# Optimization experiments

Measured on AMD Instinct MI355X. Metric: run time of the kernel, lower is better.

## Reference

```python
import jax, jax.numpy as jnp
import numpy as np

B, S, E = 4, 2048, 1024
H, Dh = 16, 64


def setup_inputs() -> dict:
    key = jax.random.key(0)
    ks = jax.random.split(key, 9)
    scale_in = 1.0 / np.sqrt(E)
    scale_out = 1.0 / np.sqrt(H * Dh)
    x = jax.random.normal(ks[0], (B, S, E), dtype=jnp.float32)
    # Per-head projection weights stacked over heads: [H, E, Dh]
    Wq = jax.random.uniform(ks[1], (H, E, Dh), jnp.float32, -scale_in, scale_in)
    bq = jax.random.uniform(ks[2], (H, Dh), jnp.float32, -scale_in, scale_in)
    Wk = jax.random.uniform(ks[3], (H, E, Dh), jnp.float32, -scale_in, scale_in)
    bk = jax.random.uniform(ks[4], (H, Dh), jnp.float32, -scale_in, scale_in)
    Wv = jax.random.uniform(ks[5], (H, E, Dh), jnp.float32, -scale_in, scale_in)
    bv = jax.random.uniform(ks[6], (H, Dh), jnp.float32, -scale_in, scale_in)
    # Output projection: [H*Dh, E]
    Wo = jax.random.uniform(ks[7], (H * Dh, E), jnp.float32, -scale_out, scale_out)
    bo = jax.random.uniform(ks[8], (E,), jnp.float32, -scale_out, scale_out)
    return {"x": x, "Wq": Wq, "bq": bq, "Wk": Wk, "bk": bk,
            "Wv": Wv, "bv": bv, "Wo": Wo, "bo": bo}


def reference(x, Wq, bq, Wk, bk, Wv, bv, Wo, bo):
    # Per-head linear projections, batched over heads: [B, H, S, Dh]
    q = jnp.einsum('bse,hed->bhsd', x, Wq) + bq[None, :, None, :]
    k = jnp.einsum('bse,hed->bhsd', x, Wk) + bk[None, :, None, :]
    v = jnp.einsum('bse,hed->bhsd', x, Wv) + bv[None, :, None, :]
    scale = 1.0 / jnp.sqrt(jnp.asarray(Dh, dtype=x.dtype))
    scores = jnp.einsum('bhsd,bhtd->bhst', q, k) * scale  # [B, H, S, S]
    weights = jax.nn.softmax(scores, axis=-1)
    z = jnp.einsum('bhst,bhtd->bhsd', weights, v)  # [B, H, S, Dh]
    # Concat heads in module order: [B, S, H*Dh]
    z = jnp.transpose(z, (0, 2, 1, 3)).reshape(B, S, H * Dh)
    return z @ Wo + bo
```

## Files before the change

kernel.cpp:

```cpp
#include <hip/hip_runtime.h>
#include <hip/hip_bf16.h>

#define B_  4
#define S_  2048
#define E_  1024
#define H_  16
#define DH_ 64
#define M_  (B_*S_)
#define HD_ (H_*DH_)

typedef unsigned short u16;
typedef __attribute__((ext_vector_type(8))) __bf16 bf16x8;
typedef __attribute__((ext_vector_type(4))) __bf16 bf16x4;
typedef __attribute__((ext_vector_type(4))) float  f32x4;

#if __has_builtin(__builtin_amdgcn_exp2f)
#define EXP2F __builtin_amdgcn_exp2f
#else
#define EXP2F __builtin_exp2f
#endif

#define QSCALE 0.18033688011112042f

__device__ __forceinline__ void g2l16(const void* g, void* l) {
  __builtin_amdgcn_global_load_lds(
      (const __attribute__((address_space(1))) void*)g,
      (__attribute__((address_space(3))) void*)l, 16, 0, 0);
}

__device__ __forceinline__ u16 f2bf(float f) {
  union { float f; unsigned u; } v; v.f = f;
  unsigned r = v.u + 0x7FFFu + ((v.u >> 16) & 1u);
  return (u16)(r >> 16);
}

__global__ __launch_bounds__(256) void prep_kernel(
    const float* __restrict__ x, const float* __restrict__ Wq,
    const float* __restrict__ Wk, const float* __restrict__ Wv,
    const float* __restrict__ Wo,
    u16* __restrict__ xb, u16* __restrict__ wqkvT, u16* __restrict__ woT) {
  __shared__ u16 tile[64][66];
  const int blk = blockIdx.x, tid = threadIdx.x;
  if (blk < 8192) {
    int i = blk * 256 + tid;
    float4 v = ((const float4*)x)[i];
    ushort4 o;
    o.x = f2bf(v.x); o.y = f2bf(v.y); o.z = f2bf(v.z); o.w = f2bf(v.w);
    ((ushort4*)xb)[i] = o;
  } else if (blk < 8960) {
    int b2 = blk - 8192;
    int p = b2 >> 8, h = (b2 >> 4) & 15, e0 = (b2 & 15) * 64;
    const float* src = (p == 0 ? Wq : (p == 1 ? Wk : Wv)) + h * (E_ * DH_);
#pragma unroll
    for (int r = 0; r < 16; ++r) {
      int idx = r * 256 + tid;
      int el = idx >> 6, d = idx & 63;
      tile[el][d] = f2bf(src[(e0 + el) * DH_ + d]);
    }
    __syncthreads();
    u16* dst = wqkvT + (p * HD_ + h * DH_) * E_;
#pragma unroll
    for (int r = 0; r < 16; ++r) {
      int idx = r * 256 + tid;
      int d = idx >> 6, el = idx & 63;
      dst[d * E_ + e0 + el] = tile[el][d];
    }
  } else {
    int b3 = blk - 8960;
    int c0 = (b3 >> 4) * 64, e0 = (b3 & 15) * 64;
#pragma unroll
    for (int r = 0; r < 16; ++r) {
      int idx = r * 256 + tid;
      int cl = idx >> 6, el = idx & 63;
      tile[cl][el] = f2bf(Wo[(c0 + cl) * E_ + e0 + el]);
    }
    __syncthreads();
#pragma unroll
    for (int r = 0; r < 16; ++r) {
      int idx = r * 256 + tid;
      int er = idx >> 6, cl = idx & 63;
      woT[(e0 + er) * HD_ + c0 + cl] = tile[cl][er];
    }
  }
}

__global__ __launch_bounds__(256) void gemm_qkv_kernel(
    const u16* __restrict__ A, const u16* __restrict__ Bt,
    const float* __restrict__ b0, const float* __restrict__ b1,
    const float* __restrict__ b2,
    u16* __restrict__ oQ, u16* __restrict__ oK, u16* __restrict__ oV) {
  constexpr int K = 1024;
  __shared__ __align__(16) u16 smem[2 * 128 * 64];
  u16* As = smem;
  u16* Bs = smem + 128 * 64;
  const int tid = threadIdx.x;
  const int lane = tid & 63, wv = tid >> 6;
  const int wm = (wv >> 1) * 64, wn = (wv & 1) * 64;
  const int q4 = lane >> 4, lm = lane & 15;
  const int tileM = blockIdx.y * 128, tileN = blockIdx.x * 128;

  const u16* gA[4]; const u16* gB[4]; u16* lA[4]; u16* lB[4];
#pragma unroll
  for (int rr = 0; rr < 4; ++rr) {
    int c = rr * 256 + tid;
    int r = c >> 3, sw = ((c & 7) ^ (r & 7)) * 8;
    gA[rr] = A + (size_t)(tileM + r) * K + sw;
    gB[rr] = Bt + (size_t)(tileN + r) * K + sw;
    lA[rr] = As + c * 8;
    lB[rr] = Bs + c * 8;
  }

  f32x4 acc[4][4] = {};

  int aoff[2][4], boff[2][4];
#pragma unroll
  for (int ks = 0; ks < 2; ++ks) {
#pragma unroll
    for (int i = 0; i < 4; ++i) {
      int ra = wm + i * 16 + lm;
      aoff[ks][i] = ra * 64 + (((ks * 4 + q4) ^ (ra & 7)) * 8);
      int rb = wn + i * 16 + lm;
      boff[ks][i] = rb * 64 + (((ks * 4 + q4) ^ (rb & 7)) * 8);
    }
  }

  for (int k0 = 0; k0 < K; k0 += 64) {
#pragma unroll
    for (int rr = 0; rr < 4; ++rr) {
      g2l16(gA[rr] + k0, lA[rr]);
      g2l16(gB[rr] + k0, lB[rr]);
    }
    __syncthreads();
#pragma unroll
    for (int ks = 0; ks < 2; ++ks) {
      bf16x8 af[4], bf[4];
#pragma unroll
      for (int i = 0; i < 4; ++i) af[i] = *(const bf16x8*)(As + aoff[ks][i]);
#pragma unroll
      for (int j = 0; j < 4; ++j) bf[j] = *(const bf16x8*)(Bs + boff[ks][j]);
#pragma unroll
      for (int i = 0; i < 4; ++i)
#pragma unroll
        for (int j = 0; j < 4; ++j)
          acc[i][j] = __builtin_amdgcn_mfma_f32_16x16x32_bf16(af[i], bf[j], acc[i][j], 0, 0, 0);
    }
    __syncthreads();
  }

  u16* TT = smem;
  const int ccb = tileN & 1023;
  const int proj = tileN >> 10;
  const float scl = (proj == 0 ? QSCALE : 1.0f);
  const float* bp = (proj == 0 ? b0 : (proj == 1 ? b1 : b2));
#pragma unroll
  for (int j = 0; j < 4; ++j) {
    int ncl = wn + j * 16 + lm;
    float bs = bp[ccb + ncl];
#pragma unroll
    for (int i = 0; i < 4; ++i) {
      int m0 = wm + i * 16 + q4 * 4;
      f32x4 vv;
#pragma unroll
      for (int r = 0; r < 4; ++r) vv[r] = (acc[i][j][r] + bs) * scl;
      bf16x4 ov = __builtin_convertvector(vv, bf16x4);
      if (proj < 2) {
        ushort4 us = *(ushort4*)&ov;
        TT[(m0 + 0) * 128 + (ncl ^ (8 * ((m0 + 0) & 15)))] = us.x;
        TT[(m0 + 1) * 128 + (ncl ^ (8 * ((m0 + 1) & 15)))] = us.y;
        TT[(m0 + 2) * 128 + (ncl ^ (8 * ((m0 + 2) & 15)))] = us.z;
        TT[(m0 + 3) * 128 + (ncl ^ (8 * ((m0 + 3) & 15)))] = us.w;
      } else {
        *(bf16x4*)(TT + ncl * 128 + (m0 ^ (8 * (ncl & 15)))) = ov;
      }
    }
  }
  __syncthreads();
  if (proj < 2) {
    u16* optr = (proj == 0 ? oQ : oK);
#pragma unroll
    for (int rr = 0; rr < 8; ++rr) {
      int seg = rr * 256 + tid;
      int ml = seg >> 4, sc = (seg & 15) * 8;
      uint4 val = *(const uint4*)(TT + ml * 128 + (sc ^ (8 * (ml & 15))));
      *(uint4*)(optr + (size_t)(tileM + ml) * 1024 + ccb + sc) = val;
    }
  } else {
    const int bb = tileM >> 11, s0 = tileM & 2047;
#pragma unroll
    for (int rr = 0; rr < 8; ++rr) {
      int seg = rr * 256 + tid;
      int ccl = seg >> 4, sc = (seg & 15) * 8;
      int cc = ccb + ccl;
      int hh = cc >> 6, dd = cc & 63;
      uint4 val = *(const uint4*)(TT + ccl * 128 + (sc ^ (8 * (ccl & 15))));
      *(uint4*)(oV + ((size_t)(bb * 16 + hh) * 64 + dd) * 2048 + s0 + sc) = val;
    }
  }
}

__global__ __launch_bounds__(256) void gemm_o_kernel(
    const u16* __restrict__ A, const u16* __restrict__ Bt,
    const float* __restrict__ bo, float* __restrict__ oF) {
  constexpr int K = 1024;
  __shared__ __align__(16) u16 smem[(64 + 128) * 64];
  u16* As = smem;
  u16* Bs = smem + 64 * 64;
  const int tid = threadIdx.x;
  const int lane = tid & 63, wv = tid >> 6;
  const int wm = (wv >> 1) * 32, wn = (wv & 1) * 64;
  const int q4 = lane >> 4, lm = lane & 15;

  const int bid = blockIdx.x;
  const int wg = (bid & 7) * 128 + (bid >> 3);
  const int tileN = (wg & 7) * 128, tileM = (wg >> 3) * 64;

  const u16* gA[2]; const u16* gB[4]; u16* lA[2]; u16* lB[4];
#pragma unroll
  for (int rr = 0; rr < 2; ++rr) {
    int c = rr * 256 + tid;
    int r = c >> 3, sw = ((c & 7) ^ (r & 7)) * 8;
    gA[rr] = A + (size_t)(tileM + r) * K + sw;
    lA[rr] = As + c * 8;
  }
#pragma unroll
  for (int rr = 0; rr < 4; ++rr) {
    int c = rr * 256 + tid;
    int r = c >> 3, sw = ((c & 7) ^ (r & 7)) * 8;
    gB[rr] = Bt + (size_t)(tileN + r) * K + sw;
    lB[rr] = Bs + c * 8;
  }

  f32x4 acc[2][4] = {};

  int aoff[2][2], boff[2][4];
#pragma unroll
  for (int ks = 0; ks < 2; ++ks) {
#pragma unroll
    for (int i = 0; i < 2; ++i) {
      int ra = wm + i * 16 + lm;
      aoff[ks][i] = ra * 64 + (((ks * 4 + q4) ^ (ra & 7)) * 8);
    }
#pragma unroll
    for (int j = 0; j < 4; ++j) {
      int rb = wn + j * 16 + lm;
      boff[ks][j] = rb * 64 + (((ks * 4 + q4) ^ (rb & 7)) * 8);
    }
  }

  for (int k0 = 0; k0 < K; k0 += 64) {
#pragma unroll
    for (int rr = 0; rr < 2; ++rr) g2l16(gA[rr] + k0, lA[rr]);
#pragma unroll
    for (int rr = 0; rr < 4; ++rr) g2l16(gB[rr] + k0, lB[rr]);
    __syncthreads();
#pragma unroll
    for (int ks = 0; ks < 2; ++ks) {
      bf16x8 af[2], bf[4];
#pragma unroll
      for (int i = 0; i < 2; ++i) af[i] = *(const bf16x8*)(As + aoff[ks][i]);
#pragma unroll
      for (int j = 0; j < 4; ++j) bf[j] = *(const bf16x8*)(Bs + boff[ks][j]);
#pragma unroll
      for (int i = 0; i < 2; ++i)
#pragma unroll
        for (int j = 0; j < 4; ++j)
          acc[i][j] = __builtin_amdgcn_mfma_f32_16x16x32_bf16(af[i], bf[j], acc[i][j], 0, 0, 0);
    }
    __syncthreads();
  }

#pragma unroll
  for (int j = 0; j < 4; ++j) {
    int n = tileN + wn + j * 16 + lm;
    float bs = bo[n];
#pragma unroll
    for (int i = 0; i < 2; ++i) {
      int m0 = tileM + wm + i * 16 + q4 * 4;
#pragma unroll
      for (int r = 0; r < 4; ++r) oF[(m0 + r) * HD_ + n] = acc[i][j][r] + bs;
    }
  }
}

__global__ __launch_bounds__(256, 2) void flash_kernel(
    const u16* __restrict__ Q, const u16* __restrict__ Kb,
    const u16* __restrict__ Vt, u16* __restrict__ Z) {
  __shared__ __align__(16) u16 Ks[2][64 * 64];
  __shared__ __align__(16) u16 Vs[2][64 * 64];
  const int tid = threadIdx.x, lane = tid & 63, wv = tid >> 6;
  const int q4 = lane >> 4, lm = lane & 15;

  const int bid = blockIdx.x;
  const int bh = bid >> 4, qt = bid & 15;
  const int b = bh >> 4, h = bh & 15;

  const u16* qbase = Q + ((size_t)(b * S_ + qt * 128)) * HD_ + h * DH_;
  const u16* kbase = Kb + (size_t)b * S_ * HD_ + h * DH_;
  const u16* vbase = Vt + ((size_t)(b * H_ + h)) * DH_ * S_;
  u16* zbase = Z + ((size_t)(b * S_ + qt * 128)) * HD_ + h * DH_;

  const int c0 = tid,       r0 = c0 >> 3, s0 = ((c0 & 7) ^ (r0 & 7)) * 8;
  const int c1 = tid + 256, r1 = c1 >> 3, s1 = ((c1 & 7) ^ (r1 & 7)) * 8;
  const int kr0 = ((r0 >> 4) & 1) * 32 + ((r0 >> 2) & 3) * 8 + (r0 >> 5) * 4 + (r0 & 3);
  const int kr1 = ((r1 >> 4) & 1) * 32 + ((r1 >> 2) & 3) * 8 + (r1 >> 5) * 4 + (r1 & 3);

  bf16x8 qf[2][2];
#pragma unroll
  for (int qs = 0; qs < 2; ++qs)
#pragma unroll
    for (int dc = 0; dc < 2; ++dc)
      qf[qs][dc] = *(const bf16x8*)(qbase + (wv * 32 + qs * 16 + lm) * HD_ + dc * 32 + q4 * 8);

  const bf16x8 ones = {(__bf16)1.f, (__bf16)1.f, (__bf16)1.f, (__bf16)1.f,
                       (__bf16)1.f, (__bf16)1.f, (__bf16)1.f, (__bf16)1.f};

  const int base0 = lm * 64 + ((q4 ^ (lm & 7)) * 8);
  const int base1 = lm * 64 + (((4 + q4) ^ (lm & 7)) * 8);

  f32x4 oacc[2][4] = {};
  f32x4 liacc[2] = {};

  {
    g2l16(kbase + kr0 * HD_ + s0, Ks[0] + c0 * 8);
    g2l16(kbase + kr1 * HD_ + s1, Ks[0] + c1 * 8);
    g2l16(vbase + r0 * S_ + s0, Vs[0] + c0 * 8);
    g2l16(vbase + r1 * S_ + s1, Vs[0] + c1 * 8);
  }

  for (int t = 0; t < 32; ++t) {
    const int pb = t & 1;
    __syncthreads();
    if (t < 31) {
      const u16* kt = kbase + (size_t)(t + 1) * 64 * HD_;
      const u16* vt = vbase + (t + 1) * 64;
      g2l16(kt + kr0 * HD_ + s0, Ks[1 - pb] + c0 * 8);
      g2l16(kt + kr1 * HD_ + s1, Ks[1 - pb] + c1 * 8);
      g2l16(vt + r0 * S_ + s0, Vs[1 - pb] + c0 * 8);
      g2l16(vt + r1 * S_ + s1, Vs[1 - pb] + c1 * 8);
    }
    const u16* Kp = Ks[pb];
    const u16* Vp = Vs[pb];

#pragma unroll
    for (int ck = 0; ck < 2; ++ck) {
      bf16x8 ka0 = *(const bf16x8*)(Kp + ck * 1024 + base0);
      bf16x8 ka1 = *(const bf16x8*)(Kp + ck * 1024 + base1);
      bf16x8 kb0 = *(const bf16x8*)(Kp + (ck + 2) * 1024 + base0);
      bf16x8 kb1 = *(const bf16x8*)(Kp + (ck + 2) * 1024 + base1);
      bf16x8 pf[2];
#pragma unroll
      for (int qs = 0; qs < 2; ++qs) {
        f32x4 sa = {}, sb = {};
        sa = __builtin_amdgcn_mfma_f32_16x16x32_bf16(ka0, qf[qs][0], sa, 0, 0, 0);
        sa = __builtin_amdgcn_mfma_f32_16x16x32_bf16(ka1, qf[qs][1], sa, 0, 0, 0);
        sb = __builtin_amdgcn_mfma_f32_16x16x32_bf16(kb0, qf[qs][0], sb, 0, 0, 0);
        sb = __builtin_amdgcn_mfma_f32_16x16x32_bf16(kb1, qf[qs][1], sb, 0, 0, 0);
        f32x4 pa, pb2;
#pragma unroll
        for (int r = 0; r < 4; ++r) { pa[r] = EXP2F(sa[r]); pb2[r] = EXP2F(sb[r]); }
        bf16x4 la = __builtin_convertvector(pa, bf16x4);
        bf16x4 lb = __builtin_convertvector(pb2, bf16x4);
        pf[qs] = __builtin_shufflevector(la, lb, 0, 1, 2, 3, 4, 5, 6, 7);
      }
      const int vsel = ck ? base1 : base0;
      __builtin_amdgcn_s_setprio(1);
#pragma unroll
      for (int qs = 0; qs < 2; ++qs)
        liacc[qs] = __builtin_amdgcn_mfma_f32_16x16x32_bf16(pf[qs], ones, liacc[qs], 0, 0, 0);
#pragma unroll
      for (int db = 0; db < 4; ++db) {
        bf16x8 vf = *(const bf16x8*)(Vp + db * 1024 + vsel);
#pragma unroll
        for (int qs = 0; qs < 2; ++qs)
          oacc[qs][db] = __builtin_amdgcn_mfma_f32_16x16x32_bf16(pf[qs], vf, oacc[qs][db], 0, 0, 0);
      }
      __builtin_amdgcn_s_setprio(0);
    }
  }

#pragma unroll
  for (int qs = 0; qs < 2; ++qs) {
    float rin[4];
#pragma unroll
    for (int r = 0; r < 4; ++r) rin[r] = 1.f / liacc[qs][r];
#pragma unroll
    for (int db = 0; db < 4; ++db) {
      f32x4 vv;
#pragma unroll
      for (int r = 0; r < 4; ++r) vv[r] = oacc[qs][db][r] * rin[r];
      bf16x4 ov = __builtin_convertvector(vv, bf16x4);
      ushort4 us = *(ushort4*)&ov;
      int m0 = wv * 32 + qs * 16 + q4 * 4;
      zbase[(m0 + 0) * HD_ + db * 16 + lm] = us.x;
      zbase[(m0 + 1) * HD_ + db * 16 + lm] = us.y;
      zbase[(m0 + 2) * HD_ + db * 16 + lm] = us.z;
      zbase[(m0 + 3) * HD_ + db * 16 + lm] = us.w;
    }
  }
}

extern "C" void kernel_launch(void* const* d_in, const int* in_sizes, int n_in,
                              void* d_out, int out_size, void* d_ws, size_t ws_size,
                              hipStream_t stream) {
  const float* x  = (const float*)d_in[0];
  const float* Wq = (const float*)d_in[1];
  const float* bq = (const float*)d_in[2];
  const float* Wk = (const float*)d_in[3];
  const float* bk = (const float*)d_in[4];
  const float* Wv = (const float*)d_in[5];
  const float* bv = (const float*)d_in[6];
  const float* Wo = (const float*)d_in[7];
  const float* bo = (const float*)d_in[8];
  float* out = (float*)d_out;

  char* w = (char*)d_ws;
  u16*   xb    = (u16*)w;   w += (size_t)M_ * E_ * 2;
  u16*   wqkvT = (u16*)w;   w += (size_t)3 * HD_ * E_ * 2;
  u16*   woT   = (u16*)w;   w += (size_t)E_ * HD_ * 2;
  u16*   qB    = (u16*)w;   w += (size_t)M_ * HD_ * 2;
  u16*   kB    = (u16*)w;   w += (size_t)M_ * HD_ * 2;
  u16*   vT    = (u16*)w;   w += (size_t)M_ * HD_ * 2;
  u16*   zB    = (u16*)w;   w += (size_t)M_ * HD_ * 2;

  prep_kernel<<<dim3(9216), 256, 0, stream>>>(x, Wq, Wk, Wv, Wo, xb, wqkvT, woT);
  gemm_qkv_kernel<<<dim3(24, 64), 256, 0, stream>>>(xb, wqkvT, bq, bk, bv,
                                                    qB, kB, vT);
  flash_kernel<<<dim3(1024), 256, 0, stream>>>(qB, kB, vT, zB);
  gemm_o_kernel<<<dim3(1024), 256, 0, stream>>>(zB, woT, bo, out);
}
```

Before: 260.2 us.

## Rewrite QKV GEMM with 256x256 tiles, double-buffered LDS and ping-pong scheduling

The QKV projection GEMM moves from 128x128 tiles with 256 threads to 256x256 tiles with 512 threads (8 waves). It double-buffers global-to-LDS loads two stages ahead with explicit vmcnt waits, interleaves LDS fragment reads with MFMA phases using barriers and s_setprio, and remaps block IDs for L2 locality. This aims to hide global load latency and raise arithmetic intensity per LDS byte. In exchange it uses 128KB of LDS and many accumulator registers, which may limit occupancy, and the grid drops to 384 blocks.

```diff
diff --git a/kernel.cpp b/kernel.cpp
--- a/kernel.cpp
+++ b/kernel.cpp
@@ -84,68 +84,142 @@
   }
 }
 
-__global__ __launch_bounds__(256) void gemm_qkv_kernel(
+__global__ __launch_bounds__(512, 2) void gemm_qkv_kernel(
     const u16* __restrict__ A, const u16* __restrict__ Bt,
     const float* __restrict__ b0, const float* __restrict__ b1,
     const float* __restrict__ b2,
     u16* __restrict__ oQ, u16* __restrict__ oK, u16* __restrict__ oV) {
   constexpr int K = 1024;
-  __shared__ __align__(16) u16 smem[2 * 128 * 64];
-  u16* As = smem;
-  u16* Bs = smem + 128 * 64;
+  __shared__ __align__(16) u16 smem[65536];
   const int tid = threadIdx.x;
   const int lane = tid & 63, wv = tid >> 6;
-  const int wm = (wv >> 1) * 64, wn = (wv & 1) * 64;
+  const int wr = wv >> 2, wc = wv & 3;
   const int q4 = lane >> 4, lm = lane & 15;
-  const int tileM = blockIdx.y * 128, tileN = blockIdx.x * 128;
-
-  const u16* gA[4]; const u16* gB[4]; u16* lA[4]; u16* lB[4];
-#pragma unroll
-  for (int rr = 0; rr < 4; ++rr) {
-    int c = rr * 256 + tid;
-    int r = c >> 3, sw = ((c & 7) ^ (r & 7)) * 8;
-    gA[rr] = A + (size_t)(tileM + r) * K + sw;
-    gB[rr] = Bt + (size_t)(tileN + r) * K + sw;
-    lA[rr] = As + c * 8;
-    lB[rr] = Bs + c * 8;
-  }
-
-  f32x4 acc[4][4] = {};
-
-  int aoff[2][4], boff[2][4];
-#pragma unroll
-  for (int ks = 0; ks < 2; ++ks) {
+
+  const int bid = blockIdx.x;
+  const int wg = (bid & 7) * 48 + (bid >> 3);
+  const int tileN = (wg % 12) * 256;
+  const int tileM = (wg / 12) * 256;
+
+  const int sr = tid >> 3;
+  const int swz = ((tid & 7) ^ (sr & 7)) * 8;
+  const u16* gA = A + (size_t)(tileM + sr) * K + swz;
+  const u16* gB = Bt + (size_t)(tileN + sr) * K + swz;
+
+#define STG(t) do {                                                    \
+    u16* dA = smem + ((t) & 1) * 32768;                                \
+    u16* dB = dA + 16384;                                              \
+    const u16* sA = gA + (t) * 64;                                     \
+    const u16* sB = gB + (t) * 64;                                     \
+    _Pragma("unroll")                                                  \
+    for (int p = 0; p < 4; ++p) {                                      \
+      g2l16(sA + (size_t)p * 64 * K, dA + p * 4096 + tid * 8);         \
+      g2l16(sB + (size_t)p * 64 * K, dB + p * 4096 + tid * 8);         \
+    }                                                                  \
+  } while (0)
+
+  int aoffs[8], boffs[4];
+#pragma unroll
+  for (int i = 0; i < 8; ++i) {
+    int ra = wr * 128 + i * 16 + lm;
+    aoffs[i] = ra * 64 + ((q4 ^ (ra & 7)) * 8);
+  }
+#pragma unroll
+  for (int j = 0; j < 4; ++j) {
+    int rb = wc * 64 + j * 16 + lm;
+    boffs[j] = rb * 64 + ((q4 ^ (rb & 7)) * 8);
+  }
+
+  f32x4 acc[8][4] = {};
+  bf16x8 af[4][2];
+  bf16x8 bfr[4][2];
+
+  STG(0); STG(1);
+  asm volatile("s_waitcnt vmcnt(8)" ::: "memory");
+  __builtin_amdgcn_s_barrier();
+
+  for (int t = 0; t < 16; ++t) {
+    const u16* Ab = smem + (t & 1) * 32768;
+    const u16* Bb = Ab + 16384;
+
 #pragma unroll
     for (int i = 0; i < 4; ++i) {
-      int ra = wm + i * 16 + lm;
-      aoff[ks][i] = ra * 64 + (((ks * 4 + q4) ^ (ra & 7)) * 8);
-      int rb = wn + i * 16 + lm;
-      boff[ks][i] = rb * 64 + (((ks * 4 + q4) ^ (rb & 7)) * 8);
-    }
-  }
-
-  for (int k0 = 0; k0 < K; k0 += 64) {
-#pragma unroll
-    for (int rr = 0; rr < 4; ++rr) {
-      g2l16(gA[rr] + k0, lA[rr]);
-      g2l16(gB[rr] + k0, lB[rr]);
-    }
-    __syncthreads();
-#pragma unroll
-    for (int ks = 0; ks < 2; ++ks) {
-      bf16x8 af[4], bf[4];
-#pragma unroll
-      for (int i = 0; i < 4; ++i) af[i] = *(const bf16x8*)(As + aoff[ks][i]);
-#pragma unroll
-      for (int j = 0; j < 4; ++j) bf[j] = *(const bf16x8*)(Bs + boff[ks][j]);
-#pragma unroll
-      for (int i = 0; i < 4; ++i)
-#pragma unroll
-        for (int j = 0; j < 4; ++j)
-          acc[i][j] = __builtin_amdgcn_mfma_f32_16x16x32_bf16(af[i], bf[j], acc[i][j], 0, 0, 0);
-    }
-    __syncthreads();
-  }
+      af[i][0] = *(const bf16x8*)(Ab + aoffs[i]);
+      af[i][1] = *(const bf16x8*)(Ab + (aoffs[i] ^ 32));
+    }
+#pragma unroll
+    for (int j = 0; j < 2; ++j) {
+      bfr[j][0] = *(const bf16x8*)(Bb + boffs[j]);
+      bfr[j][1] = *(const bf16x8*)(Bb + (boffs[j] ^ 32));
+    }
+    __builtin_amdgcn_s_barrier();
+    __builtin_amdgcn_s_setprio(1);
+#pragma unroll
+    for (int i = 0; i < 4; ++i)
+#pragma unroll
+      for (int j = 0; j < 2; ++j) {
+        acc[i][j] = __builtin_amdgcn_mfma_f32_16x16x32_bf16(af[i][0], bfr[j][0], acc[i][j], 0, 0, 0);
+        acc[i][j] = __builtin_amdgcn_mfma_f32_16x16x32_bf16(af[i][1], bfr[j][1], acc[i][j], 0, 0, 0);
+      }
+    __builtin_amdgcn_s_setprio(0);
+    __builtin_amdgcn_s_barrier();
+
+#pragma unroll
+    for (int j = 2; j < 4; ++j) {
+      bfr[j][0] = *(const bf16x8*)(Bb + boffs[j]);
+      bfr[j][1] = *(const bf16x8*)(Bb + (boffs[j] ^ 32));
+    }
+    __builtin_amdgcn_s_barrier();
+    __builtin_amdgcn_s_setprio(1);
+#pragma unroll
+    for (int i = 0; i < 4; ++i)
+#pragma unroll
+      for (int j = 2; j < 4; ++j) {
+        acc[i][j] = __builtin_amdgcn_mfma_f32_16x16x32_bf16(af[i][0], bfr[j][0], acc[i][j], 0, 0, 0);
+        acc[i][j] = __builtin_amdgcn_mfma_f32_16x16x32_bf16(af[i][1], bfr[j][1], acc[i][j], 0, 0, 0);
+      }
+    __builtin_amdgcn_s_setprio(0);
+    __builtin_amdgcn_s_barrier();
+
+#pragma unroll
+    for (int i = 0; i < 4; ++i) {
+      af[i][0] = *(const bf16x8*)(Ab + aoffs[i + 4]);
+      af[i][1] = *(const bf16x8*)(Ab + (aoffs[i + 4] ^ 32));
+    }
+    __builtin_amdgcn_s_barrier();
+    __builtin_amdgcn_s_setprio(1);
+#pragma unroll
+    for (int i = 0; i < 4; ++i)
+#pragma unroll
+      for (int j = 2; j < 4; ++j) {
+        acc[i + 4][j] = __builtin_amdgcn_mfma_f32_16x16x32_bf16(af[i][0], bfr[j][0], acc[i + 4][j], 0, 0, 0);
+        acc[i + 4][j] = __builtin_amdgcn_mfma_f32_16x16x32_bf16(af[i][1], bfr[j][1], acc[i + 4][j], 0, 0, 0);
+      }
+    __builtin_amdgcn_s_setprio(0);
+    __builtin_amdgcn_s_barrier();
+    asm volatile("" ::: "memory");
+
+    if (t < 14) STG(t + 2);
+    __builtin_amdgcn_s_barrier();
+    __builtin_amdgcn_s_setprio(1);
+#pragma unroll
+    for (int i = 0; i < 4; ++i)
+#pragma unroll
+      for (int j = 0; j < 2; ++j) {
+        acc[i + 4][j] = __builtin_amdgcn_mfma_f32_16x16x32_bf16(af[i][0], bfr[j][0], acc[i + 4][j], 0, 0, 0);
+        acc[i + 4][j] = __builtin_amdgcn_mfma_f32_16x16x32_bf16(af[i][1], bfr[j][1], acc[i + 4][j], 0, 0, 0);
+      }
+    __builtin_amdgcn_s_setprio(0);
+    if (t < 14) {
+      asm volatile("s_waitcnt vmcnt(8)" ::: "memory");
+    } else if (t == 14) {
+      asm volatile("s_waitcnt vmcnt(0)" ::: "memory");
+    }
+    __builtin_amdgcn_s_barrier();
+  }
+#undef STG
+
+  __syncthreads();
 
   u16* TT = smem;
   const int ccb = tileN & 1023;
@@ -154,23 +228,23 @@
   const float* bp = (proj == 0 ? b0 : (proj == 1 ? b1 : b2));
 #pragma unroll
   for (int j = 0; j < 4; ++j) {
-    int ncl = wn + j * 16 + lm;
-    float bs = bp[ccb + ncl];
-#pragma unroll
-    for (int i = 0; i < 4; ++i) {
-      int m0 = wm + i * 16 + q4 * 4;
+    const int ncl = wc * 64 + j * 16 + lm;
+    const float bs = bp[ccb + ncl];
+#pragma unroll
+    for (int i = 0; i < 8; ++i) {
+      const int m0 = wr * 128 + i * 16 + q4 * 4;
       f32x4 vv;
 #pragma unroll
       for (int r = 0; r < 4; ++r) vv[r] = (acc[i][j][r] + bs) * scl;
       bf16x4 ov = __builtin_convertvector(vv, bf16x4);
       if (proj < 2) {
         ushort4 us = *(ushort4*)&ov;
-        TT[(m0 + 0) * 128 + (ncl ^ (8 * ((m0 + 0) & 15)))] = us.x;
-        TT[(m0 + 1) * 128 + (ncl ^ (8 * ((m0 + 1) & 15)))] = us.y;
-        TT[(m0 + 2) * 128 + (ncl ^ (8 * ((m0 + 2) & 15)))] = us.z;
-        TT[(m0 + 3) * 128 + (ncl ^ (8 * ((m0 + 3) & 15)))] = us.w;
+        TT[(m0 + 0) * 256 + (ncl ^ (8 * ((m0 + 0) & 15)))] = us.x;
+        TT[(m0 + 1) * 256 + (ncl ^ (8 * ((m0 + 1) & 15)))] = us.y;
+        TT[(m0 + 2) * 256 + (ncl ^ (8 * ((m0 + 2) & 15)))] = us.z;
+        TT[(m0 + 3) * 256 + (ncl ^ (8 * ((m0 + 3) & 15)))] = us.w;
       } else {
-        *(bf16x4*)(TT + ncl * 128 + (m0 ^ (8 * (ncl & 15)))) = ov;
+        *(bf16x4*)(TT + ncl * 256 + (m0 ^ (8 * (ncl & 15)))) = ov;
       }
     }
   }
@@ -178,22 +252,21 @@
   if (proj < 2) {
     u16* optr = (proj == 0 ? oQ : oK);
 #pragma unroll
-    for (int rr = 0; rr < 8; ++rr) {
-      int seg = rr * 256 + tid;
-      int ml = seg >> 4, sc = (seg & 15) * 8;
-      uint4 val = *(const uint4*)(TT + ml * 128 + (sc ^ (8 * (ml & 15))));
+    for (int it = 0; it < 16; ++it) {
+      int seg = it * 512 + tid;
+      int ml = seg >> 5, sc = (seg & 31) * 8;
+      uint4 val = *(const uint4*)(TT + ml * 256 + (sc ^ (8 * (ml & 15))));
       *(uint4*)(optr + (size_t)(tileM + ml) * 1024 + ccb + sc) = val;
     }
   } else {
-    const int bb = tileM >> 11, s0 = tileM & 2047;
-#pragma unroll
-    for (int rr = 0; rr < 8; ++rr) {
-      int seg = rr * 256 + tid;
-      int ccl = seg >> 4, sc = (seg & 15) * 8;
-      int cc = ccb + ccl;
-      int hh = cc >> 6, dd = cc & 63;
-      uint4 val = *(const uint4*)(TT + ccl * 128 + (sc ^ (8 * (ccl & 15))));
-      *(uint4*)(oV + ((size_t)(bb * 16 + hh) * 64 + dd) * 2048 + s0 + sc) = val;
+    const int bb = tileM >> 11, s0v = tileM & 2047;
+#pragma unroll
+    for (int it = 0; it < 16; ++it) {
+      int seg = it * 512 + tid;
+      int ccl = seg >> 5, sc = (seg & 31) * 8;
+      uint4 val = *(const uint4*)(TT + ccl * 256 + (sc ^ (8 * (ccl & 15))));
+      int cc = ccb + ccl, hh = cc >> 6, dd = cc & 63;
+      *(uint4*)(oV + ((size_t)(bb * 16 + hh) * 64 + dd) * 2048 + s0v + sc) = val;
     }
   }
 }
@@ -423,8 +496,7 @@
   u16*   zB    = (u16*)w;   w += (size_t)M_ * HD_ * 2;
 
   prep_kernel<<<dim3(9216), 256, 0, stream>>>(x, Wq, Wk, Wv, Wo, xb, wqkvT, woT);
-  gemm_qkv_kernel<<<dim3(24, 64), 256, 0, stream>>>(xb, wqkvT, bq, bk, bv,
-                                                    qB, kB, vT);
+  gemm_qkv_kernel<<<dim3(384), 512, 0, stream>>>(xb, wqkvT, bq, bk, bv, qB, kB, vT);
   flash_kernel<<<dim3(1024), 256, 0, stream>>>(qB, kB, vT, zB);
   gemm_o_kernel<<<dim3(1024), 256, 0, stream>>>(zB, woT, bo, out);
 }
```

After: 281.9 us. 8.3% more time.
